# Kernel optimization log

Hardware: AMD Instinct MI355X
Metric: run time of the kernel (lower is better)

Reference implementation:

```python
import jax, jax.numpy as jnp
import numpy as np

N, E, D, H, C, L = 50000, 600000, 128, 128, 64, 3
LN_EPS = 1e-5


def setup_inputs() -> dict:
    key = jax.random.key(0)
    ks = jax.random.split(key, 6)
    x = jax.random.normal(ks[0], (N, D), jnp.float32)
    edge_index = jax.random.randint(ks[1], (2, E), 0, N, jnp.int32)
    Wg = jax.random.normal(ks[2], (L, D, H), jnp.float32) * (1.0 / np.sqrt(D))
    bg = jnp.zeros((L, H), jnp.float32)
    ln_g = jnp.ones((L, H), jnp.float32)
    ln_b = jnp.zeros((L, H), jnp.float32)
    mlp_W1 = jax.random.normal(ks[3], (D + L * H, H), jnp.float32) * (1.0 / np.sqrt(D + L * H))
    mlp_b1 = jnp.zeros((H,), jnp.float32)
    mlp_W2 = jax.random.normal(ks[4], (H, C), jnp.float32) * (1.0 / np.sqrt(H))
    mlp_b2 = jnp.zeros((C,), jnp.float32)
    return {"x": x, "edge_index": edge_index, "Wg": Wg, "bg": bg,
            "ln_g": ln_g, "ln_b": ln_b, "mlp_W1": mlp_W1, "mlp_b1": mlp_b1,
            "mlp_W2": mlp_W2, "mlp_b2": mlp_b2}


def _layer_norm(h, g, b):
    mu = jnp.mean(h, axis=-1, keepdims=True)
    var = jnp.mean((h - mu) ** 2, axis=-1, keepdims=True)
    return g * (h - mu) * jax.lax.rsqrt(var + LN_EPS) + b


def _gcn(h, W, b, src, dst, dinv):
    # GCNConv with added self-loops and symmetric normalization:
    # out = D^{-1/2} (A + I) D^{-1/2} (h W) + b
    hW = h @ W                                   # [N, H]
    coef = (dinv[src] * dinv[dst])[:, None]      # [E, 1]
    agg = jax.ops.segment_sum(hW[src] * coef, dst, num_segments=N)
    agg = agg + hW * (dinv * dinv)[:, None]      # self-loop term
    return agg + b


def reference(x, edge_index, Wg, bg, ln_g, ln_b, mlp_W1, mlp_b1, mlp_W2, mlp_b2):
    src, dst = edge_index[0], edge_index[1]
    # degree including self-loop
    deg = jnp.ones((N,), x.dtype).at[dst].add(1.0)
    dinv = jax.lax.rsqrt(deg)
    feats = [x]
    h = x
    for i in range(L):  # small fixed layer count
        h = _gcn(h, Wg[i], bg[i], src, dst, dinv)
        h = _layer_norm(h, ln_g[i], ln_b[i])
        h = jax.nn.relu(h)
        feats.append(h)
    xc = jnp.concatenate(feats, axis=1)          # [N, D + L*H]
    z = jax.nn.relu(xc @ mlp_W1 + mlp_b1)
    z = z @ mlp_W2 + mlp_b2
    return jax.nn.softmax(z, axis=1)
```

## Files before the change

kernel.cpp:

```cpp
#include <hip/hip_runtime.h>
#include <math.h>

#define D 128
#define HH 128
#define CC 64
#define NLAYERS 3
#define LN_EPS 1e-5f

typedef __attribute__((ext_vector_type(8))) short bf16x8;
typedef __attribute__((ext_vector_type(4))) float f32x4;
typedef unsigned short u16;
typedef unsigned int u32;

__device__ __forceinline__ u16 f2bf(float f) {
    u32 u = __float_as_uint(f);
    u32 r = u + 0x7FFFu + ((u >> 16) & 1u);
    return (u16)(r >> 16);
}
__device__ __forceinline__ float bf2f(u16 h) {
    return __uint_as_float(((u32)h) << 16);
}


__global__ void k_zero_cnt(int* __restrict__ cnt, int n) {
    int i = blockIdx.x * blockDim.x + threadIdx.x;
    if (i < n) cnt[i] = 0;
}

__global__ void k_count(const int* __restrict__ dst, int* __restrict__ cnt, int E) {
    int i = blockIdx.x * blockDim.x + threadIdx.x;
    if (i < E) atomicAdd(&cnt[dst[i]], 1);
}

__global__ void k_scan_a(const int* __restrict__ cnt, int* __restrict__ rowptr,
                         int* __restrict__ bsum, int N) {
    __shared__ int s[1024];
    int tid = threadIdx.x;
    int i = blockIdx.x * 1024 + tid;
    int v = (i < N) ? cnt[i] : 0;
    s[tid] = v;
    __syncthreads();
    for (int off = 1; off < 1024; off <<= 1) {
        int t = (tid >= off) ? s[tid - off] : 0;
        __syncthreads();
        s[tid] += t;
        __syncthreads();
    }
    if (i < N) rowptr[i] = s[tid] - v;
    if (tid == 1023) bsum[blockIdx.x] = s[tid];
}

__global__ void k_scan_b(int* __restrict__ bsum, int nb) {
    int t = threadIdx.x;
    int v = (t < nb) ? bsum[t] : 0;
    int incl = v;
    for (int off = 1; off < 64; off <<= 1) {
        int u = __shfl_up(incl, off, 64);
        if (t >= off) incl += u;
    }
    if (t < nb) bsum[t] = incl - v;
}

__global__ void k_scan_c(int* __restrict__ rowptr, const int* __restrict__ bsum,
                         const int* __restrict__ cnt, float* __restrict__ dinv,
                         int* __restrict__ cursor, int N, int E) {
    int i = blockIdx.x * blockDim.x + threadIdx.x;
    if (i < N) {
        int v = rowptr[i] + bsum[i >> 10];
        rowptr[i] = v;
        cursor[i] = v;
        dinv[i] = rsqrtf(1.0f + (float)cnt[i]);
    }
    if (i == 0) rowptr[N] = E;
}

__global__ void k_scatter(const int* __restrict__ src, const int* __restrict__ dst,
                          const float* __restrict__ dinv,
                          int* __restrict__ cursor, int2* __restrict__ ecol, int E) {
    int i = blockIdx.x * blockDim.x + threadIdx.x;
    if (i < E) {
        int s = src[i], d = dst[i];
        int p = atomicAdd(&cursor[d], 1);
        float c = dinv[s] * dinv[d];
        ecol[p] = make_int2(s, __float_as_int(c));
    }
}


__global__ void k_split_x(const float* __restrict__ x, u16* __restrict__ xh,
                          u16* __restrict__ xl, int total) {
    int i = blockIdx.x * blockDim.x + threadIdx.x;
    if (i >= total) return;
    int row = i >> 7, c = i & 127;
    float v = x[i];
    u16 h = f2bf(v);
    u16 l = f2bf(v - bf2f(h));
    xh[(size_t)row * 512 + c] = h;
    xl[(size_t)row * 128 + c] = l;
}

__global__ void k_tile_w(const float* __restrict__ W, u16* __restrict__ th,
                         u16* __restrict__ tl, int KN, int nshift) {
    int idx = blockIdx.x * blockDim.x + threadIdx.x;
    if (idx >= KN) return;
    int k = idx >> nshift, n = idx & ((1 << nshift) - 1);
    int kc = k >> 5, q = (k >> 3) & 3, j = k & 7;
    float v = W[idx];
    u16 h = f2bf(v);
    int o = (((kc * 4 + q) << nshift) + n) * 8 + j;
    th[o] = h;
    if (tl) tl[o] = f2bf(v - bf2f(h));
}

template <bool SPLIT2>
__global__ __launch_bounds__(256) void k_gemm_lf(
    const u16* __restrict__ Ahi, int strideA, int colOff,
    const u16* __restrict__ Alo, int strideAlo,
    const u16* __restrict__ Bt, u16* __restrict__ OUTb, int N)
{
    const int tid  = threadIdx.x;
    const int lane = tid & 63;
    const int wave = tid >> 6;
    const int wr   = wave & 1;
    const int wc   = wave >> 1;
    const int quad = lane >> 4;
    const int l15  = lane & 15;
    const int row0 = blockIdx.x * 64;

    const u16* pAh[2];
    const u16* pAl[2];
    #pragma unroll
    for (int i = 0; i < 2; ++i) {
        int r = row0 + wr * 32 + i * 16 + l15;
        if (r >= N) r = N - 1;
        pAh[i] = Ahi + (size_t)r * strideA + colOff + quad * 8;
        if (SPLIT2) pAl[i] = Alo + (size_t)r * strideAlo + quad * 8;
    }
    const u16* pB = Bt + ((size_t)quad * 128 + wc * 64 + l15) * 8;

    bf16x8 ah[4][2], al[4][2], bh[4][4];
    #pragma unroll
    for (int kc = 0; kc < 4; ++kc) {
        #pragma unroll
        for (int i = 0; i < 2; ++i) {
            ah[kc][i] = *(const bf16x8*)(pAh[i] + kc * 32);
            if (SPLIT2) al[kc][i] = *(const bf16x8*)(pAl[i] + kc * 32);
        }
        #pragma unroll
        for (int j = 0; j < 4; ++j)
            bh[kc][j] = *(const bf16x8*)(pB + (size_t)kc * 4096 + j * 128);
    }

    f32x4 acc[2][4];
    #pragma unroll
    for (int i = 0; i < 2; ++i)
        #pragma unroll
        for (int j = 0; j < 4; ++j)
            #pragma unroll
            for (int r = 0; r < 4; ++r) acc[i][j][r] = 0.f;

    #pragma unroll
    for (int kc = 0; kc < 4; ++kc)
        #pragma unroll
        for (int i = 0; i < 2; ++i)
            #pragma unroll
            for (int j = 0; j < 4; ++j) {
                acc[i][j] = __builtin_amdgcn_mfma_f32_16x16x32_bf16(ah[kc][i], bh[kc][j], acc[i][j], 0, 0, 0);
                if (SPLIT2)
                    acc[i][j] = __builtin_amdgcn_mfma_f32_16x16x32_bf16(al[kc][i], bh[kc][j], acc[i][j], 0, 0, 0);
            }

    #pragma unroll
    for (int i = 0; i < 2; ++i)
        #pragma unroll
        for (int j = 0; j < 4; ++j) {
            int col = wc * 64 + j * 16 + l15;
            #pragma unroll
            for (int r = 0; r < 4; ++r) {
                int grow = row0 + wr * 32 + i * 16 + quad * 4 + r;
                if (grow < N)
                    OUTb[(size_t)grow * 128 + col] = f2bf(acc[i][j][r]);
            }
        }
}

__global__ __launch_bounds__(256) void k_mlp_fused(
    const u16* __restrict__ xcH, const u16* __restrict__ xl,
    const u16* __restrict__ B1t, const float* __restrict__ b1,
    const u16* __restrict__ W2h, const u16* __restrict__ W2l,
    const float* __restrict__ b2, float* __restrict__ out, int N)
{
    __shared__ float sAcc[32 * 132];
    __shared__ u16 sZh[32 * 128];
    __shared__ u16 sZl[32 * 128];

    const int tid  = threadIdx.x;
    const int lane = tid & 63;
    const int wave = tid >> 6;
    const int wc   = wave & 1;
    const int kg   = wave >> 1;
    const int quad = lane >> 4;
    const int l15  = lane & 15;
    const int row0 = blockIdx.x * 32;

    const u16* pAh[2];
    const u16* pAl[2];
    #pragma unroll
    for (int f = 0; f < 2; ++f) {
        int r = row0 + f * 16 + l15;
        if (r >= N) r = N - 1;
        pAh[f] = xcH + (size_t)r * 512 + quad * 8;
        pAl[f] = xl  + (size_t)r * 128 + quad * 8;
    }
    const u16* pB = B1t + ((size_t)quad * 128 + wc * 64 + l15) * 8;

    f32x4 acc[2][4];
    #pragma unroll
    for (int f = 0; f < 2; ++f)
        #pragma unroll
        for (int j = 0; j < 4; ++j)
            #pragma unroll
            for (int r = 0; r < 4; ++r) acc[f][j][r] = 0.f;

    bf16x8 abuf[3][2], bbuf[3][4];
    #define LOADI(t, s)                                                          \
        {                                                                        \
            const int g = kg * 10 + (t);                                         \
            const int hi = (g < 16);                                             \
            const int bk = hi ? g : g - 16;                                      \
            _Pragma("unroll")                                                    \
            for (int f = 0; f < 2; ++f) {                                        \
                const u16* pa = hi ? (pAh[f] + g * 32)                           \
                                   : (pAl[f] + (g - 16) * 32);                   \
                abuf[s][f] = *(const bf16x8*)pa;                                 \
            }                                                                    \
            _Pragma("unroll")                                                    \
            for (int j = 0; j < 4; ++j)                                          \
                bbuf[s][j] = *(const bf16x8*)(pB + (size_t)bk * 4096 + j * 128); \
        }
    LOADI(0, 0)
    LOADI(1, 1)
    #pragma unroll
    for (int t = 0; t < 10; ++t) {
        if (t + 2 < 10) {
            const int s = (t + 2) % 3;
            LOADI(t + 2, s)
        }
        const int u = t % 3;
        #pragma unroll
        for (int f = 0; f < 2; ++f)
            #pragma unroll
            for (int j = 0; j < 4; ++j)
                acc[f][j] = __builtin_amdgcn_mfma_f32_16x16x32_bf16(abuf[u][f], bbuf[u][j], acc[f][j], 0, 0, 0);
    }
    #undef LOADI

    if (kg == 1) {
        #pragma unroll
        for (int f = 0; f < 2; ++f)
            #pragma unroll
            for (int jt = 0; jt < 4; ++jt) {
                int col = wc * 64 + jt * 16 + l15;
                #pragma unroll
                for (int r = 0; r < 4; ++r) {
                    int row = f * 16 + quad * 4 + r;
                    sAcc[row * 132 + col] = acc[f][jt][r];
                }
            }
    }
    __syncthreads();
    if (kg == 0) {
        #pragma unroll
        for (int jt = 0; jt < 4; ++jt) {
            int col = wc * 64 + jt * 16 + l15;
            float bv = b1[col];
            int qq = col >> 3, jj = col & 7;
            #pragma unroll
            for (int f = 0; f < 2; ++f) {
                #pragma unroll
                for (int rr = 0; rr < 4; ++rr) {
                    int row = f * 16 + quad * 4 + rr;
                    float v = fmaxf(acc[f][jt][rr] + sAcc[row * 132 + col] + bv, 0.f);
                    u16 h = f2bf(v);
                    sZh[(qq * 32 + row) * 8 + jj] = h;
                    sZl[(qq * 32 + row) * 8 + jj] = f2bf(v - bf2f(h));
                }
            }
        }
    }
    __syncthreads();

    if (kg == 0) {
        f32x4 oacc[4];
        #pragma unroll
        for (int j = 0; j < 4; ++j)
            #pragma unroll
            for (int r = 0; r < 4; ++r) oacc[j][r] = 0.f;

        #pragma unroll
        for (int kc = 0; kc < 4; ++kc) {
            int qq = kc * 4 + quad;
            bf16x8 zh = *(const bf16x8*)&sZh[(qq * 32 + wc * 16 + l15) * 8];
            bf16x8 zl = *(const bf16x8*)&sZl[(qq * 32 + wc * 16 + l15) * 8];
            #pragma unroll
            for (int jt = 0; jt < 4; ++jt) {
                int n = jt * 16 + l15;
                bf16x8 wh = *(const bf16x8*)&W2h[(qq * 64 + n) * 8];
                bf16x8 wl = *(const bf16x8*)&W2l[(qq * 64 + n) * 8];
                oacc[jt] = __builtin_amdgcn_mfma_f32_16x16x32_bf16(zh, wh, oacc[jt], 0, 0, 0);
                oacc[jt] = __builtin_amdgcn_mfma_f32_16x16x32_bf16(zh, wl, oacc[jt], 0, 0, 0);
                oacc[jt] = __builtin_amdgcn_mfma_f32_16x16x32_bf16(zl, wh, oacc[jt], 0, 0, 0);
            }
        }

        #pragma unroll
        for (int jt = 0; jt < 4; ++jt) {
            float bv = b2[jt * 16 + l15];
            #pragma unroll
            for (int r = 0; r < 4; ++r) oacc[jt][r] += bv;
        }
        #pragma unroll
        for (int r = 0; r < 4; ++r) {
            float m = fmaxf(fmaxf(oacc[0][r], oacc[1][r]), fmaxf(oacc[2][r], oacc[3][r]));
            #pragma unroll
            for (int mask = 8; mask; mask >>= 1) m = fmaxf(m, __shfl_xor(m, mask, 64));
            float p0 = __expf(oacc[0][r] - m);
            float p1 = __expf(oacc[1][r] - m);
            float p2 = __expf(oacc[2][r] - m);
            float p3 = __expf(oacc[3][r] - m);
            float s = p0 + p1 + p2 + p3;
            #pragma unroll
            for (int mask = 8; mask; mask >>= 1) s += __shfl_xor(s, mask, 64);
            float inv = 1.0f / s;
            int grow = row0 + wc * 16 + quad * 4 + r;
            if (grow < N) {
                float* o = out + (size_t)grow * CC + l15;
                o[0]  = p0 * inv;
                o[16] = p1 * inv;
                o[32] = p2 * inv;
                o[48] = p3 * inv;
            }
        }
    }
}

__global__ __launch_bounds__(256, 8) void k_agg_ln(
    const u16* __restrict__ hWb,
    const int* __restrict__ rowptr, const int2* __restrict__ ecol,
    const float* __restrict__ dinv,
    const float* __restrict__ bg, const float* __restrict__ g,
    const float* __restrict__ b,
    u16* __restrict__ outHi, int N)
{
    const int lane = threadIdx.x & 63;
    const int f0 = lane * 2;

    const float bgx = bg[f0], bgy = bg[f0 + 1];
    const float gx  = g[f0],  gy  = g[f0 + 1];
    const float bx  = b[f0],  by  = b[f0 + 1];

    const int nwaves = gridDim.x * 4;
    for (int wid = blockIdx.x * 4 + (threadIdx.x >> 6); wid < N; wid += nwaves) {
        float di = dinv[wid];
        float sc = di * di;

        u32 hv = *(const u32*)(hWb + (size_t)wid * HH + f0);
        float ax  = bf2f((u16)hv) * sc;
        float ay  = bf2f((u16)(hv >> 16)) * sc;
        float ax1 = 0.f, ay1 = 0.f, ax2 = 0.f, ay2 = 0.f, ax3 = 0.f, ay3 = 0.f;

        int e0 = rowptr[wid];
        int e1 = rowptr[wid + 1];
        int e = e0;
        for (; e + 8 <= e1; e += 8) {
            int2 p[8];
            u32  v[8];
            #pragma unroll
            for (int t = 0; t < 8; ++t) p[t] = ecol[e + t];
            #pragma unroll
            for (int t = 0; t < 8; ++t)
                v[t] = *(const u32*)(hWb + (size_t)p[t].x * HH + f0);
            #pragma unroll
            for (int t = 0; t < 8; ++t) {
                float c = __int_as_float(p[t].y);
                float vx = bf2f((u16)v[t]) * c;
                float vy = bf2f((u16)(v[t] >> 16)) * c;
                switch (t & 3) {
                    case 0: ax  += vx; ay  += vy; break;
                    case 1: ax1 += vx; ay1 += vy; break;
                    case 2: ax2 += vx; ay2 += vy; break;
                    default: ax3 += vx; ay3 += vy; break;
                }
            }
        }
        for (; e + 4 <= e1; e += 4) {
            int2 p0 = ecol[e];
            int2 p1 = ecol[e + 1];
            int2 p2 = ecol[e + 2];
            int2 p3 = ecol[e + 3];
            u32 v0 = *(const u32*)(hWb + (size_t)p0.x * HH + f0);
            u32 v1 = *(const u32*)(hWb + (size_t)p1.x * HH + f0);
            u32 v2 = *(const u32*)(hWb + (size_t)p2.x * HH + f0);
            u32 v3 = *(const u32*)(hWb + (size_t)p3.x * HH + f0);
            ax  += bf2f((u16)v0) * __int_as_float(p0.y);  ay  += bf2f((u16)(v0 >> 16)) * __int_as_float(p0.y);
            ax1 += bf2f((u16)v1) * __int_as_float(p1.y);  ay1 += bf2f((u16)(v1 >> 16)) * __int_as_float(p1.y);
            ax2 += bf2f((u16)v2) * __int_as_float(p2.y);  ay2 += bf2f((u16)(v2 >> 16)) * __int_as_float(p2.y);
            ax3 += bf2f((u16)v3) * __int_as_float(p3.y);  ay3 += bf2f((u16)(v3 >> 16)) * __int_as_float(p3.y);
        }
        for (; e < e1; ++e) {
            int2 p = ecol[e];
            u32 v = *(const u32*)(hWb + (size_t)p.x * HH + f0);
            float c = __int_as_float(p.y);
            ax += bf2f((u16)v) * c;
            ay += bf2f((u16)(v >> 16)) * c;
        }
        ax += ax1 + ax2 + ax3;
        ay += ay1 + ay2 + ay3;
        ax += bgx;
        ay += bgy;

        float ssum = ax + ay;
        #pragma unroll
        for (int off = 32; off; off >>= 1) ssum += __shfl_xor(ssum, off, 64);
        float mu = ssum * (1.0f / 128.0f);
        float dx = ax - mu, dy = ay - mu;
        float vsum = dx * dx + dy * dy;
        #pragma unroll
        for (int off = 32; off; off >>= 1) vsum += __shfl_xor(vsum, off, 64);
        float rstd = rsqrtf(vsum * (1.0f / 128.0f) + LN_EPS);

        float ox = fmaxf(gx * dx * rstd + bx, 0.f);
        float oy = fmaxf(gy * dy * rstd + by, 0.f);

        *(u32*)&outHi[(size_t)wid * 512 + f0] = (u32)f2bf(ox) | ((u32)f2bf(oy) << 16);
    }
}

extern "C" void kernel_launch(void* const* d_in, const int* in_sizes, int n_in,
                              void* d_out, int out_size, void* d_ws, size_t ws_size,
                              hipStream_t stream) {
    const float* x   = (const float*)d_in[0];
    const int*   ei  = (const int*)  d_in[1];
    const float* Wg  = (const float*)d_in[2];
    const float* bg  = (const float*)d_in[3];
    const float* lng = (const float*)d_in[4];
    const float* lnb = (const float*)d_in[5];
    const float* W1  = (const float*)d_in[6];
    const float* b1  = (const float*)d_in[7];
    const float* W2  = (const float*)d_in[8];
    const float* b2  = (const float*)d_in[9];
    float* out = (float*)d_out;

    const int N = in_sizes[0] / D;
    const int E = in_sizes[1] / 2;
    const int* srcp = ei;
    const int* dstp = ei + E;

    char* ws = (char*)d_ws;
    size_t off = 0;
    auto alloc = [&](size_t bytes) -> void* {
        void* p = ws + off;
        off += (bytes + 511) & ~(size_t)511;
        return p;
    };
    int*   cnt    = (int*)  alloc((size_t)N * 4);
    int*   rowptr = (int*)  alloc((size_t)(N + 1) * 4);
    int*   cursor = (int*)  alloc((size_t)N * 4);
    int*   bsum   = (int*)  alloc(64 * 4);
    int2*  ecol   = (int2*) alloc((size_t)E * 8);
    float* dinv   = (float*)alloc((size_t)N * 4);
    u16*   hWb    = (u16*)  alloc((size_t)N * HH * 2);
    u16*   xcH    = (u16*)  alloc((size_t)N * 512 * 2);
    u16*   xl     = (u16*)  alloc((size_t)N * 128 * 2);
    u16*   WgtH   = (u16*)  alloc((size_t)NLAYERS * D * HH * 2);
    u16*   W1tH   = (u16*)  alloc((size_t)(D + NLAYERS * HH) * HH * 2);
    u16*   W2tH   = (u16*)  alloc((size_t)HH * CC * 2);
    u16*   W2tL   = (u16*)  alloc((size_t)HH * CC * 2);

    const int B = 256;
    const int gN = (N + B - 1) / B;
    const int gE = (E + B - 1) / B;
    const int nsb = (N + 1023) / 1024;

    k_zero_cnt<<<gN, B, 0, stream>>>(cnt, N);
    k_count<<<gE, B, 0, stream>>>(dstp, cnt, E);
    k_scan_a<<<nsb, 1024, 0, stream>>>(cnt, rowptr, bsum, N);
    k_scan_b<<<1, 64, 0, stream>>>(bsum, nsb);
    k_scan_c<<<gN, B, 0, stream>>>(rowptr, bsum, cnt, dinv, cursor, N, E);
    k_scatter<<<gE, B, 0, stream>>>(srcp, dstp, dinv, cursor, ecol, E);

    k_split_x<<<(N * D + B - 1) / B, B, 0, stream>>>(x, xcH, xl, N * D);
    k_tile_w<<<(NLAYERS * D * HH + B - 1) / B, B, 0, stream>>>(Wg, WgtH, nullptr,
                                                               NLAYERS * D * HH, 7);
    k_tile_w<<<((D + NLAYERS * HH) * HH + B - 1) / B, B, 0, stream>>>(W1, W1tH, nullptr,
                                                                      (D + NLAYERS * HH) * HH, 7);
    k_tile_w<<<(HH * CC + B - 1) / B, B, 0, stream>>>(W2, W2tH, W2tL, HH * CC, 6);

    const int gemmBlocks = (N + 63) / 64;
    const int mlpBlocks  = (N + 31) / 32;
    const int aggBlocks  = 2048;

    for (int l = 0; l < NLAYERS; ++l) {
        if (l == 0)
            k_gemm_lf<true><<<gemmBlocks, B, 0, stream>>>(xcH, 512, 0, xl, 128,
                                                          WgtH, hWb, N);
        else
            k_gemm_lf<false><<<gemmBlocks, B, 0, stream>>>(xcH, 512, l * HH, nullptr, 0,
                                                           WgtH + (size_t)l * D * HH, hWb, N);
        k_agg_ln<<<aggBlocks, B, 0, stream>>>(hWb, rowptr, ecol, dinv,
                                              bg + (size_t)l * HH,
                                              lng + (size_t)l * HH,
                                              lnb + (size_t)l * HH,
                                              xcH + (size_t)(l + 1) * HH, N);
    }

    k_mlp_fused<<<mlpBlocks, B, 0, stream>>>(xcH, xl, W1tH, b1,
                                             W2tH, W2tL, b2, out, N);
}
```

Before: 333.7 us.

## Drop split-bf16 low part of x and fuse prep kernels into one launch

Removes the hi/lo bf16 split of the input features, so the first-layer GEMM and the MLP's first GEMM use a single bf16 MFMA pass over x instead of two, and the xl buffer is no longer written or read. The zero-count, x conversion and three weight-tiling kernels are merged into one prep kernel, and the small block-sum scan is folded into scan_c. The aim is to cut MFMA work, memory traffic and launch overhead, at the cost of lower precision on the raw input features.

```diff
diff --git a/kernel.cpp b/kernel.cpp
--- a/kernel.cpp
+++ b/kernel.cpp
@@ -21,11 +21,48 @@
     return __uint_as_float(((u32)h) << 16);
 }
 
-
-__global__ void k_zero_cnt(int* __restrict__ cnt, int n) {
+__global__ void k_prep(const float* __restrict__ x, u16* __restrict__ xh,
+                       const float* __restrict__ Wg, u16* __restrict__ WgtH,
+                       const float* __restrict__ W1, u16* __restrict__ W1tH,
+                       const float* __restrict__ W2, u16* __restrict__ W2tH,
+                       u16* __restrict__ W2tL,
+                       int* __restrict__ cnt, int N)
+{
     int i = blockIdx.x * blockDim.x + threadIdx.x;
-    if (i < n) cnt[i] = 0;
-}
+    if (i < N) { cnt[i] = 0; return; }
+    i -= N;
+    int nx = N * D;
+    if (i < nx) {
+        int row = i >> 7, c = i & 127;
+        xh[(size_t)row * 512 + c] = f2bf(x[i]);
+        return;
+    }
+    i -= nx;
+    if (i < NLAYERS * D * HH) {
+        int k = i >> 7, n = i & 127;
+        int kc = k >> 5, q = (k >> 3) & 3, j = k & 7;
+        WgtH[(((kc * 4 + q) << 7) + n) * 8 + j] = f2bf(Wg[i]);
+        return;
+    }
+    i -= NLAYERS * D * HH;
+    if (i < (D + NLAYERS * HH) * HH) {
+        int k = i >> 7, n = i & 127;
+        int kc = k >> 5, q = (k >> 3) & 3, j = k & 7;
+        W1tH[(((kc * 4 + q) << 7) + n) * 8 + j] = f2bf(W1[i]);
+        return;
+    }
+    i -= (D + NLAYERS * HH) * HH;
+    if (i < HH * CC) {
+        int k = i >> 6, n = i & 63;
+        int kc = k >> 5, q = (k >> 3) & 3, j = k & 7;
+        float v = W2[i];
+        u16 h = f2bf(v);
+        int o = (((kc * 4 + q) << 6) + n) * 8 + j;
+        W2tH[o] = h;
+        W2tL[o] = f2bf(v - bf2f(h));
+    }
+}
+
 
 __global__ void k_count(const int* __restrict__ dst, int* __restrict__ cnt, int E) {
     int i = blockIdx.x * blockDim.x + threadIdx.x;
@@ -50,23 +87,25 @@
     if (tid == 1023) bsum[blockIdx.x] = s[tid];
 }
 
-__global__ void k_scan_b(int* __restrict__ bsum, int nb) {
-    int t = threadIdx.x;
-    int v = (t < nb) ? bsum[t] : 0;
-    int incl = v;
-    for (int off = 1; off < 64; off <<= 1) {
-        int u = __shfl_up(incl, off, 64);
-        if (t >= off) incl += u;
-    }
-    if (t < nb) bsum[t] = incl - v;
-}
-
 __global__ void k_scan_c(int* __restrict__ rowptr, const int* __restrict__ bsum,
                          const int* __restrict__ cnt, float* __restrict__ dinv,
-                         int* __restrict__ cursor, int N, int E) {
+                         int* __restrict__ cursor, int N, int E, int nsb) {
+    __shared__ int sb[64];
+    if (threadIdx.x < 64) {
+        int t = threadIdx.x;
+        int v = (t < nsb) ? bsum[t] : 0;
+        int incl = v;
+        #pragma unroll
+        for (int off = 1; off < 64; off <<= 1) {
+            int u = __shfl_up(incl, off, 64);
+            if (t >= off) incl += u;
+        }
+        sb[t] = incl - v;
+    }
+    __syncthreads();
     int i = blockIdx.x * blockDim.x + threadIdx.x;
     if (i < N) {
-        int v = rowptr[i] + bsum[i >> 10];
+        int v = rowptr[i] + sb[i >> 10];
         rowptr[i] = v;
         cursor[i] = v;
         dinv[i] = rsqrtf(1.0f + (float)cnt[i]);
@@ -86,36 +125,8 @@
     }
 }
 
-
-__global__ void k_split_x(const float* __restrict__ x, u16* __restrict__ xh,
-                          u16* __restrict__ xl, int total) {
-    int i = blockIdx.x * blockDim.x + threadIdx.x;
-    if (i >= total) return;
-    int row = i >> 7, c = i & 127;
-    float v = x[i];
-    u16 h = f2bf(v);
-    u16 l = f2bf(v - bf2f(h));
-    xh[(size_t)row * 512 + c] = h;
-    xl[(size_t)row * 128 + c] = l;
-}
-
-__global__ void k_tile_w(const float* __restrict__ W, u16* __restrict__ th,
-                         u16* __restrict__ tl, int KN, int nshift) {
-    int idx = blockIdx.x * blockDim.x + threadIdx.x;
-    if (idx >= KN) return;
-    int k = idx >> nshift, n = idx & ((1 << nshift) - 1);
-    int kc = k >> 5, q = (k >> 3) & 3, j = k & 7;
-    float v = W[idx];
-    u16 h = f2bf(v);
-    int o = (((kc * 4 + q) << nshift) + n) * 8 + j;
-    th[o] = h;
-    if (tl) tl[o] = f2bf(v - bf2f(h));
-}
-
-template <bool SPLIT2>
 __global__ __launch_bounds__(256) void k_gemm_lf(
-    const u16* __restrict__ Ahi, int strideA, int colOff,
-    const u16* __restrict__ Alo, int strideAlo,
+    const u16* __restrict__ A, int colOff,
     const u16* __restrict__ Bt, u16* __restrict__ OUTb, int N)
 {
     const int tid  = threadIdx.x;
@@ -127,25 +138,21 @@
     const int l15  = lane & 15;
     const int row0 = blockIdx.x * 64;
 
-    const u16* pAh[2];
-    const u16* pAl[2];
+    const u16* pA[2];
     #pragma unroll
     for (int i = 0; i < 2; ++i) {
         int r = row0 + wr * 32 + i * 16 + l15;
         if (r >= N) r = N - 1;
-        pAh[i] = Ahi + (size_t)r * strideA + colOff + quad * 8;
-        if (SPLIT2) pAl[i] = Alo + (size_t)r * strideAlo + quad * 8;
+        pA[i] = A + (size_t)r * 512 + colOff + quad * 8;
     }
     const u16* pB = Bt + ((size_t)quad * 128 + wc * 64 + l15) * 8;
 
-    bf16x8 ah[4][2], al[4][2], bh[4][4];
+    bf16x8 ah[4][2], bh[4][4];
     #pragma unroll
     for (int kc = 0; kc < 4; ++kc) {
         #pragma unroll
-        for (int i = 0; i < 2; ++i) {
-            ah[kc][i] = *(const bf16x8*)(pAh[i] + kc * 32);
-            if (SPLIT2) al[kc][i] = *(const bf16x8*)(pAl[i] + kc * 32);
-        }
+        for (int i = 0; i < 2; ++i)
+            ah[kc][i] = *(const bf16x8*)(pA[i] + kc * 32);
         #pragma unroll
         for (int j = 0; j < 4; ++j)
             bh[kc][j] = *(const bf16x8*)(pB + (size_t)kc * 4096 + j * 128);
@@ -164,11 +171,8 @@
         #pragma unroll
         for (int i = 0; i < 2; ++i)
             #pragma unroll
-            for (int j = 0; j < 4; ++j) {
+            for (int j = 0; j < 4; ++j)
                 acc[i][j] = __builtin_amdgcn_mfma_f32_16x16x32_bf16(ah[kc][i], bh[kc][j], acc[i][j], 0, 0, 0);
-                if (SPLIT2)
-                    acc[i][j] = __builtin_amdgcn_mfma_f32_16x16x32_bf16(al[kc][i], bh[kc][j], acc[i][j], 0, 0, 0);
-            }
 
     #pragma unroll
     for (int i = 0; i < 2; ++i)
@@ -185,7 +189,7 @@
 }
 
 __global__ __launch_bounds__(256) void k_mlp_fused(
-    const u16* __restrict__ xcH, const u16* __restrict__ xl,
+    const u16* __restrict__ xcH,
     const u16* __restrict__ B1t, const float* __restrict__ b1,
     const u16* __restrict__ W2h, const u16* __restrict__ W2l,
     const float* __restrict__ b2, float* __restrict__ out, int N)
@@ -203,14 +207,12 @@
     const int l15  = lane & 15;
     const int row0 = blockIdx.x * 32;
 
-    const u16* pAh[2];
-    const u16* pAl[2];
+    const u16* pA[2];
     #pragma unroll
     for (int f = 0; f < 2; ++f) {
         int r = row0 + f * 16 + l15;
         if (r >= N) r = N - 1;
-        pAh[f] = xcH + (size_t)r * 512 + quad * 8;
-        pAl[f] = xl  + (size_t)r * 128 + quad * 8;
+        pA[f] = xcH + (size_t)r * 512 + quad * 8;
     }
     const u16* pB = B1t + ((size_t)quad * 128 + wc * 64 + l15) * 8;
 
@@ -225,24 +227,19 @@
     bf16x8 abuf[3][2], bbuf[3][4];
     #define LOADI(t, s)                                                          \
         {                                                                        \
-            const int g = kg * 10 + (t);                                         \
-            const int hi = (g < 16);                                             \
-            const int bk = hi ? g : g - 16;                                      \
+            const int g = kg * 8 + (t);                                          \
             _Pragma("unroll")                                                    \
-            for (int f = 0; f < 2; ++f) {                                        \
-                const u16* pa = hi ? (pAh[f] + g * 32)                           \
-                                   : (pAl[f] + (g - 16) * 32);                   \
-                abuf[s][f] = *(const bf16x8*)pa;                                 \
-            }                                                                    \
+            for (int f = 0; f < 2; ++f)                                          \
+                abuf[s][f] = *(const bf16x8*)(pA[f] + g * 32);                   \
             _Pragma("unroll")                                                    \
             for (int j = 0; j < 4; ++j)                                          \
-                bbuf[s][j] = *(const bf16x8*)(pB + (size_t)bk * 4096 + j * 128); \
+                bbuf[s][j] = *(const bf16x8*)(pB + (size_t)g * 4096 + j * 128);  \
         }
     LOADI(0, 0)
     LOADI(1, 1)
     #pragma unroll
-    for (int t = 0; t < 10; ++t) {
-        if (t + 2 < 10) {
+    for (int t = 0; t < 8; ++t) {
+        if (t + 2 < 8) {
             const int s = (t + 2) % 3;
             LOADI(t + 2, s)
         }
@@ -471,42 +468,31 @@
     float* dinv   = (float*)alloc((size_t)N * 4);
     u16*   hWb    = (u16*)  alloc((size_t)N * HH * 2);
     u16*   xcH    = (u16*)  alloc((size_t)N * 512 * 2);
-    u16*   xl     = (u16*)  alloc((size_t)N * 128 * 2);
     u16*   WgtH   = (u16*)  alloc((size_t)NLAYERS * D * HH * 2);
     u16*   W1tH   = (u16*)  alloc((size_t)(D + NLAYERS * HH) * HH * 2);
     u16*   W2tH   = (u16*)  alloc((size_t)HH * CC * 2);
     u16*   W2tL   = (u16*)  alloc((size_t)HH * CC * 2);
 
     const int B = 256;
-    const int gN = (N + B - 1) / B;
     const int gE = (E + B - 1) / B;
     const int nsb = (N + 1023) / 1024;
 
-    k_zero_cnt<<<gN, B, 0, stream>>>(cnt, N);
+    const int prepTotal = N + N * D + NLAYERS * D * HH
+                        + (D + NLAYERS * HH) * HH + HH * CC;
+    k_prep<<<(prepTotal + B - 1) / B, B, 0, stream>>>(x, xcH, Wg, WgtH, W1, W1tH,
+                                                      W2, W2tH, W2tL, cnt, N);
     k_count<<<gE, B, 0, stream>>>(dstp, cnt, E);
     k_scan_a<<<nsb, 1024, 0, stream>>>(cnt, rowptr, bsum, N);
-    k_scan_b<<<1, 64, 0, stream>>>(bsum, nsb);
-    k_scan_c<<<gN, B, 0, stream>>>(rowptr, bsum, cnt, dinv, cursor, N, E);
+    k_scan_c<<<(N + B - 1) / B, B, 0, stream>>>(rowptr, bsum, cnt, dinv, cursor, N, E, nsb);
     k_scatter<<<gE, B, 0, stream>>>(srcp, dstp, dinv, cursor, ecol, E);
-
-    k_split_x<<<(N * D + B - 1) / B, B, 0, stream>>>(x, xcH, xl, N * D);
-    k_tile_w<<<(NLAYERS * D * HH + B - 1) / B, B, 0, stream>>>(Wg, WgtH, nullptr,
-                                                               NLAYERS * D * HH, 7);
-    k_tile_w<<<((D + NLAYERS * HH) * HH + B - 1) / B, B, 0, stream>>>(W1, W1tH, nullptr,
-                                                                      (D + NLAYERS * HH) * HH, 7);
-    k_tile_w<<<(HH * CC + B - 1) / B, B, 0, stream>>>(W2, W2tH, W2tL, HH * CC, 6);
 
     const int gemmBlocks = (N + 63) / 64;
     const int mlpBlocks  = (N + 31) / 32;
     const int aggBlocks  = 2048;
 
     for (int l = 0; l < NLAYERS; ++l) {
-        if (l == 0)
-            k_gemm_lf<true><<<gemmBlocks, B, 0, stream>>>(xcH, 512, 0, xl, 128,
-                                                          WgtH, hWb, N);
-        else
-            k_gemm_lf<false><<<gemmBlocks, B, 0, stream>>>(xcH, 512, l * HH, nullptr, 0,
-                                                           WgtH + (size_t)l * D * HH, hWb, N);
+        k_gemm_lf<<<gemmBlocks, B, 0, stream>>>(xcH, l * HH,
+                                                WgtH + (size_t)l * D * HH, hWb, N);
         k_agg_ln<<<aggBlocks, B, 0, stream>>>(hWb, rowptr, ecol, dinv,
                                               bg + (size_t)l * HH,
                                               lng + (size_t)l * HH,
@@ -514,6 +500,6 @@
                                               xcH + (size_t)(l + 1) * HH, N);
     }
 
-    k_mlp_fused<<<mlpBlocks, B, 0, stream>>>(xcH, xl, W1tH, b1,
+    k_mlp_fused<<<mlpBlocks, B, 0, stream>>>(xcH, W1tH, b1,
                                              W2tH, W2tL, b2, out, N);
 }
```

New measurement: 316.2 us. 1.06x faster.
